# Kernel tuning notes

Hardware: AMD Instinct MI355X
Metric: run time of the kernel (lower is better)

The kernel has to match this reference:

```python
import jax, jax.numpy as jnp
import numpy as np
from math import sqrt

IMG_SIZE = 512
FMAP = IMG_SIZE // 32            # 16
RATIOS = (1.0 / 3.0, 0.5, 1.0, 2.0, 3.0)
SCALE = 0.35
N_CLASSES = 21                   # class 0 = background
MIN_SCORE = 0.01
MAX_OVERLAP = 0.45
BATCH = 16


def make_anchors():
    # mirrors DetectionBaseline.create_anchors (cx, cy, w, h in [0,1])
    anchors = []
    for i in range(FMAP):
        for j in range(FMAP):
            cx = (j + 0.5) / FMAP
            cy = (i + 0.5) / FMAP
            for r in RATIOS:
                anchors.append([cx, cy, SCALE * sqrt(r), SCALE / sqrt(r)])
    return jnp.clip(jnp.asarray(anchors, dtype=jnp.float32), 0.0, 1.0)


def setup_inputs() -> dict:
    key = jax.random.key(0)
    k1, k2 = jax.random.split(key)
    A = FMAP * FMAP * len(RATIOS)  # 1280 anchors
    return {
        "predicted_locs": jax.random.normal(k1, (BATCH, A, 4), dtype=jnp.float32),
        "predicted_scores": jax.random.normal(k2, (BATCH, A, N_CLASSES), dtype=jnp.float32),
        "anchors": make_anchors(),
        "top_k": 200,
    }


def _pairwise_iou(boxes):
    # boxes: [B, A, 4] xyxy -> iou [B, A, A]
    area = (boxes[..., 2] - boxes[..., 0]) * (boxes[..., 3] - boxes[..., 1])
    lt = jnp.maximum(boxes[:, :, None, :2], boxes[:, None, :, :2])
    rb = jnp.minimum(boxes[:, :, None, 2:], boxes[:, None, :, 2:])
    wh = jnp.clip(rb - lt, 0.0, None)
    inter = wh[..., 0] * wh[..., 1]
    union = area[:, :, None] + area[:, None, :] - inter
    return inter / union


def reference(predicted_locs, predicted_scores, anchors, top_k):
    B, A, C = predicted_scores.shape
    Cf = C - 1  # foreground classes
    scores = jax.nn.softmax(predicted_scores, axis=2)  # [B, A, C]

    # standard SSD decode (gcxgcywh -> cxcywh -> xyxy)
    cxcy = predicted_locs[..., :2] * anchors[:, 2:] / 10.0 + anchors[:, :2]
    wh = jnp.exp(predicted_locs[..., 2:] / 5.0) * anchors[:, 2:]
    boxes = jnp.concatenate([cxcy - wh / 2.0, cxcy + wh / 2.0], axis=-1)  # [B, A, 4]

    iou = _pairwise_iou(boxes)  # [B, A, A], shared across classes

    cls_scores = jnp.transpose(scores[:, :, 1:], (0, 2, 1))  # [B, Cf, A]
    valid = cls_scores > MIN_SCORE
    order = jnp.argsort(-cls_scores, axis=-1)  # per-class descending score order

    bi = jnp.arange(B)[:, None]   # [B, 1]
    ci = jnp.arange(Cf)[None, :]  # [1, Cf]

    def step(suppress, idx_r):
        # idx_r: [B, Cf] anchor index processed at this rank
        row = iou[bi, idx_r, :] > MAX_OVERLAP            # [B, Cf, A]
        active = (~suppress[bi, ci, idx_r]) & valid[bi, ci, idx_r]  # [B, Cf]
        new = jnp.where(active[..., None], suppress | row, suppress)
        # original sets suppress[box] = 0 after suppressing its overlaps
        new = new.at[bi, ci, idx_r].set(jnp.where(active, False, new[bi, ci, idx_r]))
        return new, None

    suppress0 = jnp.zeros((B, Cf, A), dtype=bool)
    suppress, _ = jax.lax.scan(step, suppress0, jnp.transpose(order, (2, 0, 1)))
    keep = (~suppress) & valid  # [B, Cf, A]

    # gather top_k detections per image across (class, anchor)
    masked = jnp.where(keep, cls_scores, -1.0).reshape(B, Cf * A)
    topv, topi = jax.lax.top_k(masked, top_k)  # [B, top_k]
    cls_idx = topi // A + 1
    anc_idx = topi % A
    det_valid = topv > 0.0
    out_scores = jnp.where(det_valid, topv, 0.0)
    out_labels = jnp.where(det_valid, cls_idx, 0)
    out_boxes = jnp.where(det_valid[..., None], boxes[bi, anc_idx, :], 0.0)
    return out_boxes, out_labels, out_scores
```

## Files before the change

### kernel.cpp

```cpp
#include <hip/hip_runtime.h>
#include <stdint.h>


#define A_N     1280
#define CF      20
#define NC      21
#define B_N     16
#define TOPK    200
#define THREADS 256
#define CTHREADS 512
#define SORT_N  2048
#define CH      128

#define KEYS_BYTES   (B_N * CF * TOPK * 8)
#define BOX_OFF      KEYS_BYTES
#define MS_OFF       (BOX_OFF + B_N * A_N * 16)
#define RANKS_OFF    (MS_OFF + B_N * A_N * 8)
#define WS_B_BYTES   RANKS_OFF
#define WS_A_BYTES   (RANKS_OFF + (size_t)B_N * CF * A_N * 2)

static __device__ __forceinline__ uint64_t pack_key(float sc, uint32_t idx) {
    return ((uint64_t)(uint32_t)(~__float_as_uint(sc)) << 32) | (uint64_t)idx;
}

static __device__ __forceinline__ float box_area(const float4 v) {
    return (v.z - v.x) * (v.w - v.y);
}

static __device__ __forceinline__ bool iou_gt(const float4 a, const float aarea,
                                              const float4 b, const float barea) {
    const float lx = fmaxf(a.x, b.x);
    const float ly = fmaxf(a.y, b.y);
    const float rx = fminf(a.z, b.z);
    const float ry = fminf(a.w, b.w);
    const float wx = fmaxf(rx - lx, 0.0f);
    const float wy = fmaxf(ry - ly, 0.0f);
    const float inter = wx * wy;
    const float uni   = aarea + barea - inter;
    return inter / uni > 0.45f;
}

static __device__ __forceinline__ float4 decode_box(const float4 lc, const float4 an) {
    const float cx = lc.x * an.z / 10.0f + an.x;
    const float cy = lc.y * an.w / 10.0f + an.y;
    const float w  = expf(lc.z / 5.0f) * an.z;
    const float h  = expf(lc.w / 5.0f) * an.w;
    float4 v;
    v.x = cx - w / 2.0f; v.y = cy - h / 2.0f;
    v.z = cx + w / 2.0f; v.w = cy + h / 2.0f;
    return v;
}

static __device__ __forceinline__ float4 shfl_box(const float4 v, int lane) {
    float4 r;
    r.x = __shfl(v.x, lane, 64);
    r.y = __shfl(v.y, lane, 64);
    r.z = __shfl(v.z, lane, 64);
    r.w = __shfl(v.w, lane, 64);
    return r;
}

__global__ __launch_bounds__(THREADS)
void prep_kernel(const float* __restrict__ locs,
                 const float* __restrict__ scores,
                 const float* __restrict__ anchors,
                 float4* __restrict__ boxes_ws,
                 float2* __restrict__ ms_ws)
{
    const int g = blockIdx.x * THREADS + threadIdx.x;
    if (g >= B_N * A_N) return;
    const int a = g % A_N;
    boxes_ws[g] = decode_box(((const float4*)locs)[g], ((const float4*)anchors)[a]);
    const float* sp = scores + (size_t)g * NC;
    float m = sp[0];
    #pragma unroll
    for (int k = 1; k < NC; ++k) m = fmaxf(m, sp[k]);
    float sum = 0.0f;
    #pragma unroll
    for (int k = 0; k < NC; ++k) sum += expf(sp[k] - m);
    ms_ws[g] = make_float2(m, sum);
}

__global__ __launch_bounds__(THREADS)
void sort_kernel(const float* __restrict__ scores,
                 const float2* __restrict__ ms_ws,
                 unsigned short* __restrict__ ranks_ws)
{
    __shared__ uint64_t skeys[SORT_N];

    const int blk = blockIdx.x;
    const int b   = blk / CF;
    const int c   = blk % CF + 1;
    const int t   = threadIdx.x;
    const int l   = t & 63;
    const int w   = t >> 6;

    #pragma unroll
    for (int i = 0; i < A_N / THREADS; ++i) {
        const int a = t + i * THREADS;
        const float2 ms = ms_ws[b * A_N + a];
        const float  sl = scores[((size_t)b * A_N + a) * NC + c];
        const float  sc = expf(sl - ms.x) / ms.y;
        skeys[a] = (sc > 0.01f) ? pack_key(sc, (uint32_t)a) : ~0ull;
    }
    for (int i = A_N + t; i < SORT_N; i += THREADS) skeys[i] = ~0ull;
    __syncthreads();

    uint64_t k[8];
    #pragma unroll
    for (int r = 0; r < 8; ++r) k[r] = skeys[(w << 9) + (r << 6) + l];

    for (int kk = 2; kk <= SORT_N; kk <<= 1) {
        for (int j = kk >> 1; j; j >>= 1) {
            if (j >= 512) {
                __syncthreads();
                #pragma unroll
                for (int r = 0; r < 8; ++r) skeys[(w << 9) + (r << 6) + l] = k[r];
                __syncthreads();
                #pragma unroll
                for (int r = 0; r < 8; ++r) {
                    const int e = (w << 9) + (r << 6) + l;
                    const uint64_t o = skeys[e ^ j];
                    const bool keep_min = (((e & j) == 0) == ((e & kk) == 0));
                    const uint64_t mn = k[r] < o ? k[r] : o;
                    const uint64_t mx = k[r] < o ? o : k[r];
                    k[r] = keep_min ? mn : mx;
                }
            } else if (j >= 64) {
                const int rb = j >> 6;
                #pragma unroll
                for (int r = 0; r < 8; ++r) {
                    if ((r & rb) == 0) {
                        const int p = r | rb;
                        const int e = (w << 9) + (r << 6) + l;
                        const bool up = ((e & kk) == 0);
                        const uint64_t x = k[r], y = k[p];
                        const uint64_t mn = x < y ? x : y;
                        const uint64_t mx = x < y ? y : x;
                        k[r] = up ? mn : mx;
                        k[p] = up ? mx : mn;
                    }
                }
            } else {
                #pragma unroll
                for (int r = 0; r < 8; ++r) {
                    const uint64_t o = (uint64_t)__shfl_xor((unsigned long long)k[r], j, 64);
                    const int e = (w << 9) + (r << 6) + l;
                    const bool keep_min = (((e & j) == 0) == ((e & kk) == 0));
                    const uint64_t mn = k[r] < o ? k[r] : o;
                    const uint64_t mx = k[r] < o ? o : k[r];
                    k[r] = keep_min ? mn : mx;
                }
            }
        }
    }
    unsigned short* const dst = ranks_ws + (size_t)blk * A_N;
    #pragma unroll
    for (int r = 0; r < 8; ++r) {
        const int e = (w << 9) + (r << 6) + l;
        if (e < A_N)
            dst[e] = (k[r] == ~0ull) ? (unsigned short)0xFFFF
                                     : (unsigned short)(k[r] & 0xFFFF);
    }
}

__global__ __launch_bounds__(CTHREADS)
void chunk_nms_kernel(const float* __restrict__ scores,
                      const float2* __restrict__ ms_ws,
                      const float4* __restrict__ boxes_ws,
                      const unsigned short* __restrict__ ranks_ws,
                      uint64_t* __restrict__ ws_keys)
{
    __shared__ unsigned short sranks[A_N];
    __shared__ float4         schunk[CH];
    __shared__ uint32_t       scolp[8][64];
    __shared__ unsigned char  sdead[CH];
    __shared__ float4         swbox[TOPK];
    __shared__ unsigned short swidx[TOPK];
    __shared__ int            sW;

    const int blk = blockIdx.x;
    const int b   = blk / CF;
    const int c   = blk % CF + 1;
    const int t   = threadIdx.x;
    const int l   = t & 63;
    const int w   = t >> 6;

    const unsigned short* const rsrc = ranks_ws + (size_t)blk * A_N;
    for (int i = t; i < A_N; i += CTHREADS) sranks[i] = rsrc[i];
    if (t == 0) sW = 0;
    __syncthreads();

    int W = 0;
    for (int cb = 0; cb < A_N; cb += CH) {
        if (sranks[cb] == 0xFFFF) break;

        if (t < CH) {
            const unsigned short rk = sranks[cb + t];
            const bool v = (rk != 0xFFFF);
            schunk[t] = v ? boxes_ws[(size_t)b * A_N + rk]
                          : make_float4(-8.f, -8.f, -8.f, -8.f);
            sdead[t]  = v ? 0 : 1;
        }
        __syncthreads();

        const float4 box_lo = schunk[l];
        const float4 box_hi = schunk[64 + l];
        const float  al = box_area(box_lo);
        const float  ah = box_area(box_hi);

        {
            const int bx = t >> 2, q = t & 3;
            const float4 bv = schunk[bx];
            const float  av = box_area(bv);
            int dead = 0;
            #pragma unroll 4
            for (int i = q; i < W; i += 4) {
                const float4 bw = swbox[i];
                dead |= iou_gt(bw, box_area(bw), bv, av) ? 1 : 0;
            }
            dead |= __shfl_xor(dead, 1, 64);
            dead |= __shfl_xor(dead, 2, 64);
            if (q == 0 && dead) sdead[bx] = 1;
        }
        __syncthreads();

        {
            const int rbase = w * 16;
            uint32_t rm = (uint32_t)__ballot(l < 16 && !sdead[rbase + l]) & 0xFFFFu;
            uint32_t part = 0;
            while (rm) {
                const int j = __ffs(rm) - 1; rm &= rm - 1;
                const int row = rbase + j;
                const float4 rowsrc = (row < 64) ? box_lo : box_hi;
                const float4 rbx = shfl_box(rowsrc, row & 63);
                const float  ra  = box_area(rbx);
                part |= (iou_gt(rbx, ra, box_lo, al) ? 1u : 0u) << j;
                part |= (iou_gt(rbx, ra, box_hi, ah) ? 0x10000u : 0u) << j;
            }
            scolp[w][l] = part;
        }
        __syncthreads();

        if (w == 0) {
            uint64_t c0 = 0, h0 = 0, c1 = 0, h1 = 0;
            #pragma unroll
            for (int ww = 0; ww < 4; ++ww) {
                const uint32_t plo = scolp[ww][l];
                const uint32_t phi = scolp[ww + 4][l];
                c0 |= (uint64_t)(plo & 0xFFFFu) << (16 * ww);
                c1 |= (uint64_t)(plo >> 16)     << (16 * ww);
                h0 |= (uint64_t)(phi & 0xFFFFu) << (16 * ww);
                h1 |= (uint64_t)(phi >> 16)     << (16 * ww);
            }
            const unsigned short rk0 = sranks[cb + l];
            const unsigned short rk1 = sranks[cb + 64 + l];
            bool a0 = !sdead[l];
            bool a1 = !sdead[64 + l];
            int Wl = W;
            while (true) {
                const unsigned long long b0 = __ballot(a0);
                const unsigned long long b1 = __ballot(a1);
                if (!(b0 | b1)) break;
                const int f = b0 ? (__ffsll(b0) - 1) : (64 + __ffsll(b1) - 1);
                if (f < 64) {
                    if (l == f)      { swidx[Wl] = rk0; swbox[Wl] = box_lo; }
                } else {
                    if (l == f - 64) { swidx[Wl] = rk1; swbox[Wl] = box_hi; }
                }
                uint32_t k0, k1;
                if (f < 64) { k0 = (uint32_t)(c0 >> f) & 1;        k1 = (uint32_t)(c1 >> f) & 1; }
                else        { k0 = (uint32_t)(h0 >> (f - 64)) & 1; k1 = (uint32_t)(h1 >> (f - 64)) & 1; }
                a0 = a0 && !k0;
                a1 = a1 && !k1;
                if (++Wl >= TOPK) break;
            }
            if (l == 0) sW = Wl;
        }
        __syncthreads();
        W = sW;
        if (W >= TOPK) break;
    }

    const uint32_t  base = (uint32_t)(c - 1) * A_N;
    uint64_t* const out  = ws_keys + ((size_t)b * CF + (c - 1)) * TOPK;
    for (int k2 = t; k2 < TOPK; k2 += CTHREADS) {
        if (k2 < W) {
            const int a = swidx[k2];
            const float2 ms = ms_ws[(size_t)b * A_N + a];
            const float  sc = expf(scores[((size_t)b * A_N + a) * NC + c] - ms.x) / ms.y;
            out[k2] = ((uint64_t)(uint32_t)(~__float_as_uint(sc)) << 32)
                    | (uint64_t)(base + (uint32_t)a);
        } else {
            out[k2] = ~0ull;
        }
    }
}

template <bool PREP>
__global__ __launch_bounds__(THREADS)
void nms_mono(const float* __restrict__ locs,
              const float* __restrict__ scores,
              const float* __restrict__ anchors,
              const float4* __restrict__ boxes_ws,
              const float2* __restrict__ ms_ws,
              uint64_t* __restrict__ ws_keys)
{
    __shared__ uint64_t      skeys[SORT_N];
    __shared__ float4        sbox[A_N];
    __shared__ float4        schunk[CH];
    __shared__ uint64_t      srow[CH][2];
    __shared__ float4        swbox[TOPK];
    __shared__ uint64_t      swkey[TOPK];
    __shared__ unsigned char sdead[CH];
    __shared__ int           sW;

    const int blk = blockIdx.x;
    const int b   = blk / CF;
    const int c   = blk % CF + 1;
    const int t   = threadIdx.x;
    const int l   = t & 63;
    const int w   = t >> 6;

    #pragma unroll
    for (int i = 0; i < A_N / THREADS; ++i) {
        const int a = t + i * THREADS;
        float4 v; float m, sum;
        if (PREP) {
            v = boxes_ws[b * A_N + a];
            const float2 ms = ms_ws[b * A_N + a];
            m = ms.x; sum = ms.y;
        } else {
            v = decode_box(((const float4*)locs)[(size_t)b * A_N + a],
                           ((const float4*)anchors)[a]);
            const float* sp = scores + ((size_t)b * A_N + a) * NC;
            m = sp[0];
            #pragma unroll
            for (int k = 1; k < NC; ++k) m = fmaxf(m, sp[k]);
            sum = 0.0f;
            #pragma unroll
            for (int k = 0; k < NC; ++k) sum += expf(sp[k] - m);
        }
        sbox[a] = v;
        const float sl = scores[((size_t)b * A_N + a) * NC + c];
        const float sc = expf(sl - m) / sum;
        skeys[a] = (sc > 0.01f) ? pack_key(sc, (uint32_t)a) : ~0ull;
    }
    for (int i = A_N + t; i < SORT_N; i += THREADS) skeys[i] = ~0ull;
    if (t == 0) sW = 0;
    __syncthreads();

    uint64_t k[8];
    #pragma unroll
    for (int r = 0; r < 8; ++r) k[r] = skeys[(w << 9) + (r << 6) + l];
    for (int kk = 2; kk <= SORT_N; kk <<= 1) {
        for (int j = kk >> 1; j; j >>= 1) {
            if (j >= 512) {
                __syncthreads();
                #pragma unroll
                for (int r = 0; r < 8; ++r) skeys[(w << 9) + (r << 6) + l] = k[r];
                __syncthreads();
                #pragma unroll
                for (int r = 0; r < 8; ++r) {
                    const int e = (w << 9) + (r << 6) + l;
                    const uint64_t o = skeys[e ^ j];
                    const bool keep_min = (((e & j) == 0) == ((e & kk) == 0));
                    const uint64_t mn = k[r] < o ? k[r] : o;
                    const uint64_t mx = k[r] < o ? o : k[r];
                    k[r] = keep_min ? mn : mx;
                }
            } else if (j >= 64) {
                const int rb = j >> 6;
                #pragma unroll
                for (int r = 0; r < 8; ++r) {
                    if ((r & rb) == 0) {
                        const int p = r | rb;
                        const int e = (w << 9) + (r << 6) + l;
                        const bool up = ((e & kk) == 0);
                        const uint64_t x = k[r], y = k[p];
                        const uint64_t mn = x < y ? x : y;
                        const uint64_t mx = x < y ? y : x;
                        k[r] = up ? mn : mx;
                        k[p] = up ? mx : mn;
                    }
                }
            } else {
                #pragma unroll
                for (int r = 0; r < 8; ++r) {
                    const uint64_t o = (uint64_t)__shfl_xor((unsigned long long)k[r], j, 64);
                    const int e = (w << 9) + (r << 6) + l;
                    const bool keep_min = (((e & j) == 0) == ((e & kk) == 0));
                    const uint64_t mn = k[r] < o ? k[r] : o;
                    const uint64_t mx = k[r] < o ? o : k[r];
                    k[r] = keep_min ? mn : mx;
                }
            }
        }
    }
    __syncthreads();
    #pragma unroll
    for (int r = 0; r < 8; ++r) skeys[(w << 9) + (r << 6) + l] = k[r];
    __syncthreads();

    int W = 0;
    for (int cb = 0; cb < SORT_N; cb += CH) {
        if (skeys[cb] == ~0ull) break;
        if (t < CH) {
            const uint64_t kc = skeys[cb + t];
            const bool v = (kc != ~0ull);
            schunk[t] = v ? sbox[(uint32_t)kc] : make_float4(-8.f, -8.f, -8.f, -8.f);
            sdead[t]  = v ? 0 : 1;
        }
        __syncthreads();
        const float4 cb0 = schunk[l];
        const float4 cb1 = schunk[64 + l];
        const float  ca0 = box_area(cb0);
        const float  ca1 = box_area(cb1);
        for (int r = w * 32; r < w * 32 + 32; ++r) {
            const float4 rbx = schunk[r];
            const float  ra  = box_area(rbx);
            const uint64_t m0 = __ballot(iou_gt(rbx, ra, cb0, ca0));
            const uint64_t m1 = __ballot(iou_gt(rbx, ra, cb1, ca1));
            if (l == 0) { srow[r][0] = m0; srow[r][1] = m1; }
        }
        {
            const int jj = t >> 1, h = t & 1;
            const float4 bj = schunk[jj];
            const float  aj = box_area(bj);
            int sup = 0;
            for (int w2 = h; w2 < W; w2 += 2) {
                const float4 bw = swbox[w2];
                if (iou_gt(bw, box_area(bw), bj, aj)) { sup = 1; break; }
            }
            sup |= __shfl_xor(sup, 1, 64);
            if (h == 0 && sup) sdead[jj] = 1;
        }
        __syncthreads();
        if (t < 64) {
            bool al0 = !sdead[t];
            bool al1 = !sdead[64 + t];
            int Wl = W;
            while (true) {
                const unsigned long long bal0 = __ballot(al0);
                const unsigned long long bal1 = __ballot(al1);
                if (!(bal0 | bal1)) break;
                const int f = bal0 ? (__ffsll(bal0) - 1) : (64 + __ffsll(bal1) - 1);
                if (t == 0) { swkey[Wl] = skeys[cb + f]; swbox[Wl] = schunk[f]; }
                const uint64_t r0 = srow[f][0];
                const uint64_t r1 = srow[f][1];
                al0 = al0 && !((r0 >> t) & 1);
                al1 = al1 && !((r1 >> t) & 1);
                if (++Wl >= TOPK) break;
            }
            if (t == 0) sW = Wl;
        }
        __syncthreads();
        W = sW;
        if (W >= TOPK) break;
    }

    const uint32_t  base = (uint32_t)(c - 1) * A_N;
    uint64_t* const out  = ws_keys + ((size_t)b * CF + (c - 1)) * TOPK;
    for (int kx = t; kx < TOPK; kx += THREADS) {
        if (kx < W) {
            const uint64_t kk2 = swkey[kx];
            out[kx] = (kk2 & 0xFFFFFFFF00000000ull) | (uint64_t)(base + (uint32_t)kk2);
        } else {
            out[kx] = ~0ull;
        }
    }
}

__global__ __launch_bounds__(THREADS)
void merge_kernel(const float* __restrict__ locs,
                  const float* __restrict__ anchors,
                  const uint64_t* __restrict__ ws_keys,
                  float* __restrict__ out)
{
    __shared__ uint64_t Abuf[20][256];
    __shared__ uint64_t Bbuf[10][256];

    const int b = blockIdx.x;
    const int t = threadIdx.x;
    const uint64_t* const in = ws_keys + (size_t)b * CF * TOPK;

    for (int e = t; e < CF * 256; e += THREADS) {
        const int c = e >> 8, i = e & 255;
        Abuf[c][i] = (i < TOPK) ? in[c * TOPK + i] : ~0ull;
    }

    uint64_t (*src)[256] = Abuf;
    uint64_t (*dst)[256] = Bbuf;
    int n = CF;
    while (n > 1) {
        const int  nm    = n >> 1;
        const bool carry = (n & 1) != 0;
        __syncthreads();
        for (int e = t; e < nm * 256; e += THREADS) {
            const int mm = e >> 8, i = e & 255;
            const uint64_t x = src[2 * mm][i];
            const uint64_t y = src[2 * mm + 1][255 - i];
            dst[mm][i] = x < y ? x : y;
        }
        if (carry)
            for (int i = t; i < 256; i += THREADS) dst[nm][i] = src[n - 1][i];
        for (int j = 128; j; j >>= 1) {
            __syncthreads();
            for (int pp = t; pp < nm * 128; pp += THREADS) {
                const int mm = pp >> 7, qq = pp & 127;
                const int i  = ((qq & ~(j - 1)) << 1) | (qq & (j - 1));
                const uint64_t x = dst[mm][i], y = dst[mm][i + j];
                if (y < x) { dst[mm][i] = y; dst[mm][i + j] = x; }
            }
        }
        uint64_t (*tmp)[256] = src; src = dst; dst = tmp;
        n = nm + (carry ? 1 : 0);
    }
    __syncthreads();

    if (t < TOPK) {
        const uint64_t k = src[0][t];
        float* const boxes_out  = out;
        float* const labels_out = out + (size_t)B_N * TOPK * 4;
        float* const scores_out = out + (size_t)B_N * TOPK * 5;
        const size_t s = (size_t)b * TOPK + t;
        if (k == ~0ull) {
            boxes_out[s * 4 + 0] = 0.0f;
            boxes_out[s * 4 + 1] = 0.0f;
            boxes_out[s * 4 + 2] = 0.0f;
            boxes_out[s * 4 + 3] = 0.0f;
            labels_out[s] = 0.0f;
            scores_out[s] = 0.0f;
        } else {
            const uint32_t flat = (uint32_t)k;
            const int cls = flat / A_N;
            const int a   = flat - cls * A_N;
            const float sc = __uint_as_float(~(uint32_t)(k >> 32));
            const float4 v = decode_box(((const float4*)locs)[(size_t)b * A_N + a],
                                        ((const float4*)anchors)[a]);
            boxes_out[s * 4 + 0] = v.x;
            boxes_out[s * 4 + 1] = v.y;
            boxes_out[s * 4 + 2] = v.z;
            boxes_out[s * 4 + 3] = v.w;
            labels_out[s] = (float)(cls + 1);
            scores_out[s] = sc;
        }
    }
}

extern "C" void kernel_launch(void* const* d_in, const int* in_sizes, int n_in,
                              void* d_out, int out_size, void* d_ws, size_t ws_size,
                              hipStream_t stream) {
    const float* locs    = (const float*)d_in[0];
    const float* scores  = (const float*)d_in[1];
    const float* anchors = (const float*)d_in[2];
    uint64_t*       ws_keys  = (uint64_t*)d_ws;
    float4*         boxes_ws = (float4*)((char*)d_ws + BOX_OFF);
    float2*         ms_ws    = (float2*)((char*)d_ws + MS_OFF);
    unsigned short* ranks_ws = (unsigned short*)((char*)d_ws + RANKS_OFF);
    float*          outp     = (float*)d_out;

    if (ws_size >= WS_A_BYTES) {
        hipLaunchKernelGGL(prep_kernel, dim3((B_N * A_N + THREADS - 1) / THREADS),
                           dim3(THREADS), 0, stream, locs, scores, anchors, boxes_ws, ms_ws);
        hipLaunchKernelGGL(sort_kernel, dim3(B_N * CF), dim3(THREADS), 0, stream,
                           scores, ms_ws, ranks_ws);
        hipLaunchKernelGGL(chunk_nms_kernel, dim3(B_N * CF), dim3(CTHREADS), 0, stream,
                           scores, ms_ws, boxes_ws, ranks_ws, ws_keys);
    } else if (ws_size >= WS_B_BYTES) {
        hipLaunchKernelGGL(prep_kernel, dim3((B_N * A_N + THREADS - 1) / THREADS),
                           dim3(THREADS), 0, stream, locs, scores, anchors, boxes_ws, ms_ws);
        hipLaunchKernelGGL((nms_mono<true>), dim3(B_N * CF), dim3(THREADS), 0, stream,
                           locs, scores, anchors, boxes_ws, ms_ws, ws_keys);
    } else {
        hipLaunchKernelGGL((nms_mono<false>), dim3(B_N * CF), dim3(THREADS), 0, stream,
                           locs, scores, anchors, boxes_ws, ms_ws, ws_keys);
    }
    hipLaunchKernelGGL(merge_kernel, dim3(B_N), dim3(THREADS), 0, stream,
                       locs, anchors, ws_keys, outp);
}
```

Baseline: 188.1 us.

## Use ballot row masks and scalar alive bitsets in chunked NMS

Boxes are now loaded straight from global memory into registers, which removes the shared chunk buffer and one barrier. Each live row's suppression mask is built with wave ballots and stored as a 64-bit row, replacing the per-lane column-bit packing. The serial greedy walk then works on uniform alive bitmasks using readlane instead of a ballot per step. Areas of kept boxes are cached so the inner loop does not recompute them. The cost is redundant global box loads, since each box is read by several threads.

```diff
diff --git a/kernel.cpp b/kernel.cpp
--- a/kernel.cpp
+++ b/kernel.cpp
@@ -58,6 +58,12 @@
     r.z = __shfl(v.z, lane, 64);
     r.w = __shfl(v.w, lane, 64);
     return r;
+}
+
+static __device__ __forceinline__ uint64_t readlane_u64(uint64_t v, int lane) {
+    const uint32_t lo = (uint32_t)__builtin_amdgcn_readlane((int)(uint32_t)v, lane);
+    const uint32_t hi = (uint32_t)__builtin_amdgcn_readlane((int)(uint32_t)(v >> 32), lane);
+    return ((uint64_t)hi << 32) | lo;
 }
 
 __global__ __launch_bounds__(THREADS)
@@ -172,10 +178,10 @@
                       uint64_t* __restrict__ ws_keys)
 {
     __shared__ unsigned short sranks[A_N];
-    __shared__ float4         schunk[CH];
-    __shared__ uint32_t       scolp[8][64];
+    __shared__ uint64_t       srow[CH][2];
     __shared__ unsigned char  sdead[CH];
     __shared__ float4         swbox[TOPK];
+    __shared__ float          swarea[TOPK];
     __shared__ unsigned short swidx[TOPK];
     __shared__ int            sW;
 
@@ -187,6 +193,7 @@
     const int w   = t >> 6;
 
     const unsigned short* const rsrc = ranks_ws + (size_t)blk * A_N;
+    const float4* const bbase = boxes_ws + (size_t)b * A_N;
     for (int i = t; i < A_N; i += CTHREADS) sranks[i] = rsrc[i];
     if (t == 0) sW = 0;
     __syncthreads();
@@ -195,85 +202,68 @@
     for (int cb = 0; cb < A_N; cb += CH) {
         if (sranks[cb] == 0xFFFF) break;
 
-        if (t < CH) {
-            const unsigned short rk = sranks[cb + t];
-            const bool v = (rk != 0xFFFF);
-            schunk[t] = v ? boxes_ws[(size_t)b * A_N + rk]
-                          : make_float4(-8.f, -8.f, -8.f, -8.f);
-            sdead[t]  = v ? 0 : 1;
-        }
-        __syncthreads();
-
-        const float4 box_lo = schunk[l];
-        const float4 box_hi = schunk[64 + l];
+        const unsigned short rk0 = sranks[cb + l];
+        const unsigned short rk1 = sranks[cb + 64 + l];
+        const float4 box_lo = (rk0 != 0xFFFF) ? bbase[rk0] : make_float4(-8.f, -8.f, -8.f, -8.f);
+        const float4 box_hi = (rk1 != 0xFFFF) ? bbase[rk1] : make_float4(-8.f, -8.f, -8.f, -8.f);
         const float  al = box_area(box_lo);
         const float  ah = box_area(box_hi);
 
         {
             const int bx = t >> 2, q = t & 3;
-            const float4 bv = schunk[bx];
+            const unsigned short rkx = sranks[cb + bx];
+            const bool valid = (rkx != 0xFFFF);
+            const float4 bv = valid ? bbase[rkx] : make_float4(-8.f, -8.f, -8.f, -8.f);
             const float  av = box_area(bv);
-            int dead = 0;
+            int dead = valid ? 0 : 1;
             #pragma unroll 4
             for (int i = q; i < W; i += 4) {
-                const float4 bw = swbox[i];
-                dead |= iou_gt(bw, box_area(bw), bv, av) ? 1 : 0;
+                dead |= iou_gt(swbox[i], swarea[i], bv, av) ? 1 : 0;
             }
             dead |= __shfl_xor(dead, 1, 64);
             dead |= __shfl_xor(dead, 2, 64);
-            if (q == 0 && dead) sdead[bx] = 1;
+            if (q == 0) sdead[bx] = (unsigned char)dead;
         }
         __syncthreads();
 
         {
             const int rbase = w * 16;
             uint32_t rm = (uint32_t)__ballot(l < 16 && !sdead[rbase + l]) & 0xFFFFu;
-            uint32_t part = 0;
             while (rm) {
                 const int j = __ffs(rm) - 1; rm &= rm - 1;
                 const int row = rbase + j;
                 const float4 rowsrc = (row < 64) ? box_lo : box_hi;
                 const float4 rbx = shfl_box(rowsrc, row & 63);
                 const float  ra  = box_area(rbx);
-                part |= (iou_gt(rbx, ra, box_lo, al) ? 1u : 0u) << j;
-                part |= (iou_gt(rbx, ra, box_hi, ah) ? 0x10000u : 0u) << j;
-            }
-            scolp[w][l] = part;
+                const uint64_t m0 = __ballot(iou_gt(rbx, ra, box_lo, al));
+                const uint64_t m1 = __ballot(iou_gt(rbx, ra, box_hi, ah));
+                if (l == 0) { srow[row][0] = m0; srow[row][1] = m1; }
+            }
         }
         __syncthreads();
 
         if (w == 0) {
-            uint64_t c0 = 0, h0 = 0, c1 = 0, h1 = 0;
-            #pragma unroll
-            for (int ww = 0; ww < 4; ++ww) {
-                const uint32_t plo = scolp[ww][l];
-                const uint32_t phi = scolp[ww + 4][l];
-                c0 |= (uint64_t)(plo & 0xFFFFu) << (16 * ww);
-                c1 |= (uint64_t)(plo >> 16)     << (16 * ww);
-                h0 |= (uint64_t)(phi & 0xFFFFu) << (16 * ww);
-                h1 |= (uint64_t)(phi >> 16)     << (16 * ww);
-            }
-            const unsigned short rk0 = sranks[cb + l];
-            const unsigned short rk1 = sranks[cb + 64 + l];
-            bool a0 = !sdead[l];
-            bool a1 = !sdead[64 + l];
+            const uint64_t r0lo = srow[l][0];
+            const uint64_t r0hi = srow[l][1];
+            const uint64_t r1lo = srow[64 + l][0];
+            const uint64_t r1hi = srow[64 + l][1];
+            uint64_t alive0 = __ballot(sdead[l] == 0);
+            uint64_t alive1 = __ballot(sdead[64 + l] == 0);
             int Wl = W;
-            while (true) {
-                const unsigned long long b0 = __ballot(a0);
-                const unsigned long long b1 = __ballot(a1);
-                if (!(b0 | b1)) break;
-                const int f = b0 ? (__ffsll(b0) - 1) : (64 + __ffsll(b1) - 1);
+            while ((alive0 | alive1) && Wl < TOPK) {
+                const int f = alive0 ? __builtin_ctzll(alive0)
+                                     : 64 + __builtin_ctzll(alive1);
                 if (f < 64) {
-                    if (l == f)      { swidx[Wl] = rk0; swbox[Wl] = box_lo; }
+                    if (l == f)      { swidx[Wl] = rk0; swbox[Wl] = box_lo; swarea[Wl] = al; }
                 } else {
-                    if (l == f - 64) { swidx[Wl] = rk1; swbox[Wl] = box_hi; }
-                }
-                uint32_t k0, k1;
-                if (f < 64) { k0 = (uint32_t)(c0 >> f) & 1;        k1 = (uint32_t)(c1 >> f) & 1; }
-                else        { k0 = (uint32_t)(h0 >> (f - 64)) & 1; k1 = (uint32_t)(h1 >> (f - 64)) & 1; }
-                a0 = a0 && !k0;
-                a1 = a1 && !k1;
-                if (++Wl >= TOPK) break;
+                    if (l == f - 64) { swidx[Wl] = rk1; swbox[Wl] = box_hi; swarea[Wl] = ah; }
+                }
+                uint64_t klo, khi;
+                if (f < 64) { klo = readlane_u64(r0lo, f);      khi = readlane_u64(r0hi, f); }
+                else        { klo = readlane_u64(r1lo, f - 64); khi = readlane_u64(r1hi, f - 64); }
+                alive0 &= ~klo;
+                alive1 &= ~khi;
+                ++Wl;
             }
             if (l == 0) sW = Wl;
         }
```

New measurement: 180.4 us. 4.1% less time.
